# Kernel tuning notes

Hardware: AMD Instinct MI355X
Metric: run time of the kernel (lower is better)

Reference implementation:

```python
import jax, jax.numpy as jnp
import numpy as np

# 20 amino-acid letters and per-residue atom counts (len(struct.atoms) - 1 in the source)
LETTERS = "ARNDCQEGHILKMFPSTWYV"
RES_LEN = {"A": 4, "R": 10, "N": 7, "D": 7, "C": 5, "Q": 8, "E": 8, "G": 3, "H": 9,
           "I": 7, "L": 7, "K": 8, "M": 7, "F": 10, "P": 6, "S": 5, "T": 6, "W": 13,
           "Y": 11, "V": 6}
BATCH = 16
N_RES = 1024       # number of residues (output 'nodes')
ATOM_DIM = 64
AMINO_DIM = 256
INDS = 1           # one trailing (3,) tensor axis


def make_metadata():
    """Deterministic protein sequence + per-letter gather indices (static numpy)."""
    rng = np.random.default_rng(42)
    seq = rng.integers(0, len(LETTERS), size=N_RES)
    lens = np.array([RES_LEN[LETTERS[s]] for s in seq])
    starts = np.concatenate([[0], np.cumsum(lens)[:-1]])  # residue_indices
    atoms = int(lens.sum())
    # group residues by letter: (residue positions, atom gather indices (n_l, L))
    groups = {}
    for li, letter in enumerate(LETTERS):
        pos = np.where(seq == li)[0]
        if len(pos) == 0:
            continue
        L = RES_LEN[letter]
        idx = starts[pos][:, None] + np.arange(L)[None, :]  # (n_l, L)
        groups[letter] = (pos, idx)
    # static row offsets of each letter's weight block inside the flat weight
    offsets, off = {}, 0
    for letter in LETTERS:
        offsets[letter] = off
        off += RES_LEN[letter] * ATOM_DIM
    return atoms, groups, offsets


def setup_inputs() -> dict:
    atoms, groups, offsets = make_metadata()
    key = jax.random.key(0)
    k1, k2 = jax.random.split(key)
    x = jax.random.normal(k1, (BATCH, atoms, ATOM_DIM, 3), dtype=jnp.float32)
    total_rows = sum(RES_LEN[l] for l in LETTERS) * ATOM_DIM  # 147*64 = 9408
    W = jax.random.normal(k2, (total_rows, AMINO_DIM), dtype=jnp.float32)
    # per-expert 1/sqrt(fan_in) init scaling
    scale = np.zeros((total_rows, 1), np.float32)
    for l in LETTERS:
        fan = RES_LEN[l] * ATOM_DIM
        scale[offsets[l]:offsets[l] + fan] = 1.0 / np.sqrt(fan)
    W = W * jnp.asarray(scale)
    return {"x": x, "W_flat": W}


def reference(x, W_flat):
    """x: (B, atoms, D, 3); W_flat: (sum_l L_l*D, amino_dim).
    Equivalent to per-residue slice -> reshape -> per-letter TensLinear -> stack,
    but grouped by letter into batched GEMMs (same math, reordered)."""
    atoms, groups, offsets = make_metadata()
    B = x.shape[0]
    out = jnp.zeros((B, N_RES, AMINO_DIM, 3), dtype=x.dtype)
    for letter, (pos, idx) in groups.items():  # fixed loop over <=20 expert types
        L = RES_LEN[letter]
        fan = L * ATOM_DIM
        g = x[:, idx]                              # (B, n_l, L, D, 3) gather
        g = g.reshape(B, len(pos), fan, 3)         # flatten residue atoms x channels
        Wl = W_flat[offsets[letter]:offsets[letter] + fan]  # (fan, amino_dim)
        y = jnp.einsum("bnki,ko->bnoi", g, Wl)     # (B, n_l, amino_dim, 3)
        out = out.at[:, pos].set(y)                # scatter back into residue order
    return out
```

## Files before the change

### kernel.cpp

```cpp
#include <hip/hip_runtime.h>
#include <hip/hip_bf16.h>
#include <cstdint>
#include <cstddef>

#define NRES 1024
#define NB 16
#define ADIM 64
#define ODIM 256
#define TOTROWS 9408

typedef __bf16 bf16x8 __attribute__((ext_vector_type(8)));
typedef float f32x4 __attribute__((ext_vector_type(4)));

struct Meta {
    uint16_t start[NRES];
    uint8_t  letter[NRES];
    int atoms;
};

constexpr int RES_LEN_A[20] = {4,10,7,7,5,8,8,3,9,7,7,8,7,10,6,5,6,13,11,6};

constexpr uint32_t ss_hash(uint32_t value, uint32_t& hc) {
    value ^= hc;
    hc *= 0x931e8875u;
    value *= hc;
    value ^= value >> 16;
    return value;
}
constexpr uint32_t ss_mix(uint32_t x, uint32_t y) {
    uint32_t r = 0xca01f9ddu * x - 0x4973f715u * y;
    r ^= r >> 16;
    return r;
}

constexpr Meta make_meta() {
    Meta m = {};
    uint32_t pool[4] = {0,0,0,0};
    uint32_t hc = 0x43b0d7e5u;
    pool[0] = ss_hash(42u, hc);
    pool[1] = ss_hash(0u, hc);
    pool[2] = ss_hash(0u, hc);
    pool[3] = ss_hash(0u, hc);
    for (int s = 0; s < 4; ++s)
        for (int d = 0; d < 4; ++d)
            if (s != d) pool[d] = ss_mix(pool[d], ss_hash(pool[s], hc));
    uint32_t hb = 0x8b51f9ddu;
    uint64_t w[8] = {};
    for (int i = 0; i < 8; ++i) {
        uint32_t dv = pool[i & 3] ^ hb;
        hb *= 0x58f38dedu;
        dv *= hb;
        dv ^= dv >> 16;
        w[i] = dv;
    }
    uint64_t s64[4] = {};
    for (int i = 0; i < 4; ++i) s64[i] = w[2*i] | (w[2*i+1] << 32);
    using u128 = unsigned __int128;
    const u128 MULT = ((u128)2549297995355413924ULL << 64) | (u128)4865540595714422341ULL;
    u128 initstate = ((u128)s64[0] << 64) | (u128)s64[1];
    u128 initseq   = ((u128)s64[2] << 64) | (u128)s64[3];
    u128 inc = (initseq << 1) | (u128)1;
    u128 state = inc;
    state += initstate;
    state = state * MULT + inc;
    bool has32 = false;
    uint32_t cached = 0;
    int atoms = 0;
    for (int i = 0; i < NRES; ++i) {
        uint32_t res = 0;
        while (true) {
            uint32_t r32;
            if (has32) { r32 = cached; has32 = false; }
            else {
                state = state * MULT + inc;
                uint64_t hi = (uint64_t)(state >> 64);
                uint64_t lo = (uint64_t)state;
                uint32_t rot = (uint32_t)(state >> 122);
                uint64_t v = hi ^ lo;
                uint64_t o64 = (v >> rot) | (v << ((64u - rot) & 63u));
                cached = (uint32_t)(o64 >> 32);
                has32 = true;
                r32 = (uint32_t)o64;
            }
            uint64_t mm = (uint64_t)r32 * 20ull;
            uint32_t leftover = (uint32_t)mm;
            if (leftover >= 16u) { res = (uint32_t)(mm >> 32); break; }
        }
        m.letter[i] = (uint8_t)res;
        m.start[i] = (uint16_t)atoms;
        atoms += RES_LEN_A[res];
    }
    m.atoms = atoms;
    return m;
}

constexpr Meta H_META = make_meta();

struct LetterTab {
    int woff[21];
    int fan[20];
};
constexpr LetterTab make_tab() {
    LetterTab t = {};
    int off = 0;
    for (int l = 0; l < 20; ++l) {
        t.woff[l] = off;
        t.fan[l] = RES_LEN_A[l] * ADIM;
        off += t.fan[l];
    }
    t.woff[20] = off;
    return t;
}

struct Perm { uint16_t p[NRES]; };
constexpr Perm make_perm() {
    int ord[20];
    for (int i = 0; i < 20; ++i) ord[i] = i;
    for (int a = 0; a < 20; ++a) {
        int best = a;
        for (int j = a + 1; j < 20; ++j)
            if (RES_LEN_A[ord[j]] > RES_LEN_A[ord[best]]) best = j;
        int t = ord[a]; ord[a] = ord[best]; ord[best] = t;
    }
    Perm pr = {};
    int n = 0;
    for (int oi = 0; oi < 20; ++oi) {
        const int l = ord[oi];
        for (int p = 0; p < NRES; ++p)
            if (H_META.letter[p] == l) pr.p[n++] = (uint16_t)p;
    }
    return pr;
}

__constant__ Meta g_meta = make_meta();
__constant__ LetterTab g_tab = make_tab();
__constant__ Perm g_perm = make_perm();

__device__ __bf16 g_Wt[(size_t)TOTROWS * ODIM];

__global__ __launch_bounds__(256) void prep_W_kernel(const float* __restrict__ W) {
    const int tid = threadIdx.x;
    const int b = blockIdx.x * 4 + (tid >> 6);
    const int lane = tid & 63;
    const int l15 = lane & 15;
    const int g4 = lane >> 4;

    int l = 0;
    while (b >= (g_tab.woff[l + 1] >> 1)) ++l;
    const int rel = b - (g_tab.woff[l] >> 1);
    const int c = rel >> 5;
    const int r32 = rel & 31;
    const int h = r32 >> 4;
    const int wv = (r32 >> 2) & 3;
    const int nt = r32 & 3;

    const int n = wv * 64 + nt * 16 + l15;
    const int kg = g_tab.woff[l] + c * 64 + h * 32 + g4 * 8;

    bf16x8 v;
    #pragma unroll
    for (int q = 0; q < 8; ++q)
        v[q] = (__bf16)W[(size_t)(kg + q) * ODIM + n];
    *(bf16x8*)&g_Wt[(size_t)b * 512 + (size_t)(l15 * 4 + g4) * 8] = v;
}

__device__ __forceinline__ void block_sync_nodrain() {
    asm volatile("s_waitcnt lgkmcnt(0)" ::: "memory");
    __builtin_amdgcn_s_barrier();
    asm volatile("" ::: "memory");
}

__global__ __launch_bounds__(512, 4) void lin_mfma_kernel(const float* __restrict__ x,
                                                          float* __restrict__ out,
                                                          int atoms) {
    const int p = g_perm.p[blockIdx.x];
    const int letter = g_meta.letter[p];
    const int start = g_meta.start[p];
    const int fan = g_tab.fan[letter];
    const __bf16* wslab = g_Wt + (size_t)g_tab.woff[letter] * ODIM;

    const int tid = threadIdx.x;
    const int lane = tid & 63;
    const int w8 = tid >> 6;
    const int l15 = lane & 15;
    const int g4 = lane >> 4;

    __shared__ __align__(16) __bf16 As[2][48][72];

    const float* xb = x + (size_t)start * 192;
    const size_t bstr = (size_t)atoms * 192;
    const int nc = fan >> 6;

    const int bl0 = tid / 48, r40 = tid - bl0 * 48;
    const int e41 = 512 + tid;
    const int bl1 = e41 / 48, r41 = e41 - bl1 * 48;
    const bool has1 = (tid < 256);

    const __bf16* wbase = wslab + (size_t)(w8 * 2) * 512 + (size_t)(l15 * 4 + g4) * 8;

    f32x4 acc[3][2];
    #pragma unroll
    for (int t = 0; t < 3; ++t)
        #pragma unroll
        for (int n = 0; n < 2; ++n)
            acc[t][n] = (f32x4){0.f, 0.f, 0.f, 0.f};

    float4 xA0, xA1, xB0, xB1;
    bf16x8 wP[4], wQ[4];

    auto LOADX = [&](int cc, float4& v0, float4& v1) {
        const size_t koff = (size_t)cc * 192;
        v0 = *(const float4*)&xb[(size_t)bl0 * bstr + koff + (size_t)r40 * 4];
        if (has1) v1 = *(const float4*)&xb[(size_t)bl1 * bstr + koff + (size_t)r41 * 4];
    };
    auto LOADW = [&](int cc, bf16x8* wf) {
        const __bf16* wc = wbase + (size_t)cc * 16384;
        #pragma unroll
        for (int h = 0; h < 2; ++h)
            #pragma unroll
            for (int ntl = 0; ntl < 2; ++ntl)
                wf[h * 2 + ntl] = *(const bf16x8*)(wc + (size_t)h * 8192 + (size_t)ntl * 512);
    };
    auto COMMIT = [&](int buf, const float4& v0, const float4& v1) {
        const float f0[4] = {v0.x, v0.y, v0.z, v0.w};
        #pragma unroll
        for (int q = 0; q < 4; ++q) {
            const int r = r40 * 4 + q, kl = r / 3, i = r - kl * 3;
            As[buf][bl0 * 3 + i][kl] = (__bf16)f0[q];
        }
        if (has1) {
            const float f1[4] = {v1.x, v1.y, v1.z, v1.w};
            #pragma unroll
            for (int q = 0; q < 4; ++q) {
                const int r = r41 * 4 + q, kl = r / 3, i = r - kl * 3;
                As[buf][bl1 * 3 + i][kl] = (__bf16)f1[q];
            }
        }
    };
    auto COMPUTE = [&](int buf, const bf16x8* wf) {
        #pragma unroll
        for (int h = 0; h < 2; ++h) {
            bf16x8 a[3];
            #pragma unroll
            for (int t = 0; t < 3; ++t)
                a[t] = *(const bf16x8*)&As[buf][t * 16 + l15][h * 32 + g4 * 8];
            #pragma unroll
            for (int ntl = 0; ntl < 2; ++ntl)
                #pragma unroll
                for (int t = 0; t < 3; ++t)
                    acc[t][ntl] = __builtin_amdgcn_mfma_f32_16x16x32_bf16(a[t], wf[h * 2 + ntl], acc[t][ntl], 0, 0, 0);
        }
    };

    LOADX(0, xA0, xA1);
    LOADX(1, xB0, xB1);
    LOADW(0, wP);
    COMMIT(0, xA0, xA1);
    if (2 < nc) LOADX(2, xA0, xA1);
    block_sync_nodrain();

    int c = 0, buf = 0;
    while (true) {
        if (c + 1 < nc) {
            LOADW(c + 1, wQ);
            COMMIT(buf ^ 1, xB0, xB1);
            if (c + 3 < nc) LOADX(c + 3, xB0, xB1);
        }
        COMPUTE(buf, wP);
        if (++c == nc) break;
        block_sync_nodrain();
        buf ^= 1;

        if (c + 1 < nc) {
            LOADW(c + 1, wP);
            COMMIT(buf ^ 1, xA0, xA1);
            if (c + 3 < nc) LOADX(c + 3, xA0, xA1);
        }
        COMPUTE(buf, wQ);
        if (++c == nc) break;
        block_sync_nodrain();
        buf ^= 1;
    }

    #pragma unroll
    for (int t = 0; t < 3; ++t)
        #pragma unroll
        for (int reg = 0; reg < 4; ++reg) {
            const int r = t * 16 + g4 * 4 + reg;
            const int bl = r / 3;
            const int i = r - bl * 3;
            #pragma unroll
            for (int ntl = 0; ntl < 2; ++ntl) {
                const int o = w8 * 32 + ntl * 16 + l15;
                out[(((size_t)bl * NRES + p) * ODIM + o) * 3 + i] = acc[t][ntl][reg];
            }
        }
}

extern "C" void kernel_launch(void* const* d_in, const int* in_sizes, int n_in,
                              void* d_out, int out_size, void* d_ws, size_t ws_size,
                              hipStream_t stream) {
    (void)n_in; (void)out_size; (void)d_ws; (void)ws_size;
    const float* x = (const float*)d_in[0];
    const float* W = (const float*)d_in[1];
    float* out = (float*)d_out;
    const int atoms = in_sizes[0] / (NB * ADIM * 3);
    prep_W_kernel<<<TOTROWS / 8, 256, 0, stream>>>(W);
    lin_mfma_kernel<<<NRES, 512, 0, stream>>>(x, out, atoms);
}
```

Before: 45.91 us.

## Stage x tiles via direct global-to-LDS async loads with double-buffered raw staging

Replaces the register-based prefetch of x (float4 loads held in registers, then committed to LDS) with global_load_lds DMA into a raw fp32 staging buffer two chunks ahead, followed by an LDS-to-LDS transpose/convert into the bf16 A tile. Weight fragments are now loaded just-in-time inside the compute loop rather than double-buffered in registers, and the launch-bounds occupancy hint is dropped. This aims to cut register pressure and VMEM-to-register latency, but adds an extra barrier per chunk, 24KB more LDS per block, and exposes weight load latency directly before the MFMAs.

```diff
diff --git a/kernel.cpp b/kernel.cpp
--- a/kernel.cpp
+++ b/kernel.cpp
@@ -164,15 +164,16 @@
     *(bf16x8*)&g_Wt[(size_t)b * 512 + (size_t)(l15 * 4 + g4) * 8] = v;
 }
 
-__device__ __forceinline__ void block_sync_nodrain() {
-    asm volatile("s_waitcnt lgkmcnt(0)" ::: "memory");
-    __builtin_amdgcn_s_barrier();
-    asm volatile("" ::: "memory");
-}
-
-__global__ __launch_bounds__(512, 4) void lin_mfma_kernel(const float* __restrict__ x,
-                                                          float* __restrict__ out,
-                                                          int atoms) {
+__device__ __forceinline__ void gload16(const void* g, void* l) {
+    __builtin_amdgcn_global_load_lds(
+        (const __attribute__((address_space(1))) uint32_t*)(uintptr_t)g,
+        (__attribute__((address_space(3))) uint32_t*)(uint32_t)(uintptr_t)l,
+        16, 0, 0);
+}
+
+__global__ __launch_bounds__(512) void lin_mfma_kernel(const float* __restrict__ x,
+                                                       float* __restrict__ out,
+                                                       int atoms) {
     const int p = g_perm.p[blockIdx.x];
     const int letter = g_meta.letter[p];
     const int start = g_meta.start[p];
@@ -185,11 +186,30 @@
     const int l15 = lane & 15;
     const int g4 = lane >> 4;
 
+    __shared__ __align__(16) uint8_t raw[2 * 12288];
     __shared__ __align__(16) __bf16 As[2][48][72];
 
     const float* xb = x + (size_t)start * 192;
-    const size_t bstr = (size_t)atoms * 192;
+    const size_t bstrB = (size_t)atoms * 768;
     const int nc = fan >> 6;
+
+    const int s0 = 2 * w8, s1 = s0 + 1;
+    const uint32_t pos0 = (uint32_t)(s0 * 1024 + lane * 16);
+    const uint32_t pos1 = (uint32_t)(s1 * 1024 + lane * 16);
+    const uint32_t b0 = pos0 / 768, o0 = pos0 - b0 * 768;
+    const uint32_t b1 = pos1 / 768, o1 = pos1 - b1 * 768;
+    const uint8_t* gsrc0 = (const uint8_t*)xb + (size_t)b0 * bstrB + o0;
+    const uint8_t* gsrc1 = (const uint8_t*)xb + (size_t)b1 * bstrB + o1;
+    uint8_t* ldst0 = raw + s0 * 1024;
+    uint8_t* ldst1 = raw + s1 * 1024;
+    const bool stager = (w8 < 6);
+
+    auto STAGE = [&](int cc) {
+        const size_t go = (size_t)cc * 768;
+        const uint32_t ro = (uint32_t)(cc & 1) * 12288u;
+        gload16(gsrc0 + go, ldst0 + ro);
+        gload16(gsrc1 + go, ldst1 + ro);
+    };
 
     const int bl0 = tid / 48, r40 = tid - bl0 * 48;
     const int e41 = 512 + tid;
@@ -205,81 +225,57 @@
         for (int n = 0; n < 2; ++n)
             acc[t][n] = (f32x4){0.f, 0.f, 0.f, 0.f};
 
-    float4 xA0, xA1, xB0, xB1;
-    bf16x8 wP[4], wQ[4];
-
-    auto LOADX = [&](int cc, float4& v0, float4& v1) {
-        const size_t koff = (size_t)cc * 192;
-        v0 = *(const float4*)&xb[(size_t)bl0 * bstr + koff + (size_t)r40 * 4];
-        if (has1) v1 = *(const float4*)&xb[(size_t)bl1 * bstr + koff + (size_t)r41 * 4];
-    };
-    auto LOADW = [&](int cc, bf16x8* wf) {
-        const __bf16* wc = wbase + (size_t)cc * 16384;
-        #pragma unroll
-        for (int h = 0; h < 2; ++h)
-            #pragma unroll
-            for (int ntl = 0; ntl < 2; ++ntl)
-                wf[h * 2 + ntl] = *(const bf16x8*)(wc + (size_t)h * 8192 + (size_t)ntl * 512);
-    };
-    auto COMMIT = [&](int buf, const float4& v0, const float4& v1) {
-        const float f0[4] = {v0.x, v0.y, v0.z, v0.w};
-        #pragma unroll
-        for (int q = 0; q < 4; ++q) {
-            const int r = r40 * 4 + q, kl = r / 3, i = r - kl * 3;
-            As[buf][bl0 * 3 + i][kl] = (__bf16)f0[q];
-        }
-        if (has1) {
-            const float f1[4] = {v1.x, v1.y, v1.z, v1.w};
+    if (stager) { STAGE(0); STAGE(1); }
+
+    for (int c = 0; c < nc; ++c) {
+        const int buf = c & 1;
+        if (stager) {
+            if (c + 1 < nc) asm volatile("s_waitcnt vmcnt(2)" ::: "memory");
+            else            asm volatile("s_waitcnt vmcnt(0)" ::: "memory");
+        }
+        __builtin_amdgcn_s_barrier();
+        asm volatile("" ::: "memory");
+
+        {
+            const uint8_t* rb = raw + (buf ? 12288 : 0);
+            const float4 v0 = *(const float4*)(rb + (size_t)tid * 16);
+            const float f0[4] = {v0.x, v0.y, v0.z, v0.w};
             #pragma unroll
             for (int q = 0; q < 4; ++q) {
-                const int r = r41 * 4 + q, kl = r / 3, i = r - kl * 3;
-                As[buf][bl1 * 3 + i][kl] = (__bf16)f1[q];
+                const int r = r40 * 4 + q, kl = r / 3, i = r - kl * 3;
+                As[buf][bl0 * 3 + i][kl] = (__bf16)f0[q];
             }
-        }
-    };
-    auto COMPUTE = [&](int buf, const bf16x8* wf) {
+            if (has1) {
+                const float4 v1 = *(const float4*)(rb + (size_t)e41 * 16);
+                const float f1[4] = {v1.x, v1.y, v1.z, v1.w};
+                #pragma unroll
+                for (int q = 0; q < 4; ++q) {
+                    const int r = r41 * 4 + q, kl = r / 3, i = r - kl * 3;
+                    As[buf][bl1 * 3 + i][kl] = (__bf16)f1[q];
+                }
+            }
+        }
+        asm volatile("s_waitcnt lgkmcnt(0)" ::: "memory");
+        __builtin_amdgcn_s_barrier();
+        asm volatile("" ::: "memory");
+
+        if (stager && c + 2 < nc) STAGE(c + 2);
+
         #pragma unroll
         for (int h = 0; h < 2; ++h) {
-            bf16x8 a[3];
+            bf16x8 a[3], wf[2];
             #pragma unroll
             for (int t = 0; t < 3; ++t)
                 a[t] = *(const bf16x8*)&As[buf][t * 16 + l15][h * 32 + g4 * 8];
+            #pragma unroll
+            for (int ntl = 0; ntl < 2; ++ntl)
+                wf[ntl] = *(const bf16x8*)(wbase + (size_t)c * 16384 + (size_t)h * 8192 + (size_t)ntl * 512);
             #pragma unroll
             for (int ntl = 0; ntl < 2; ++ntl)
                 #pragma unroll
                 for (int t = 0; t < 3; ++t)
-                    acc[t][ntl] = __builtin_amdgcn_mfma_f32_16x16x32_bf16(a[t], wf[h * 2 + ntl], acc[t][ntl], 0, 0, 0);
-        }
-    };
-
-    LOADX(0, xA0, xA1);
-    LOADX(1, xB0, xB1);
-    LOADW(0, wP);
-    COMMIT(0, xA0, xA1);
-    if (2 < nc) LOADX(2, xA0, xA1);
-    block_sync_nodrain();
-
-    int c = 0, buf = 0;
-    while (true) {
-        if (c + 1 < nc) {
-            LOADW(c + 1, wQ);
-            COMMIT(buf ^ 1, xB0, xB1);
-            if (c + 3 < nc) LOADX(c + 3, xB0, xB1);
-        }
-        COMPUTE(buf, wP);
-        if (++c == nc) break;
-        block_sync_nodrain();
-        buf ^= 1;
-
-        if (c + 1 < nc) {
-            LOADW(c + 1, wP);
-            COMMIT(buf ^ 1, xA0, xA1);
-            if (c + 3 < nc) LOADX(c + 3, xA0, xA1);
-        }
-        COMPUTE(buf, wQ);
-        if (++c == nc) break;
-        block_sync_nodrain();
-        buf ^= 1;
+                    acc[t][ntl] = __builtin_amdgcn_mfma_f32_16x16x32_bf16(a[t], wf[ntl], acc[t][ntl], 0, 0, 0);
+        }
     }
 
     #pragma unroll
```

Measured after the change: 50.23 us. 9.4% more time.
